# Optimization experiments

Hardware: AMD Instinct MI355X
Metric: run time of the kernel (lower is better)

## Reference

```python
import jax, jax.numpy as jnp
import numpy as np

N = 100_000          # ent_num
D = 256              # ent_dim
E_RAND = 3_200_000   # random edges (avg degree 32); + N self loops
NEG_SLOPE = 0.2      # LeakyReLU slope used by SpGraphAttentionLayer


def setup_inputs() -> dict:
    key = jax.random.key(0)
    k0, k1, k2, k3, k4, k5 = jax.random.split(key, 6)
    edges_rand = jax.random.randint(k0, (2, E_RAND), 0, N, dtype=jnp.int32)
    self_loops = jnp.tile(jnp.arange(N, dtype=jnp.int32)[None, :], (2, 1))
    edges = jnp.concatenate([edges_rand, self_loops], axis=1)  # [2, E]
    scale_w = 1.0 / np.sqrt(D).astype(np.float32)
    scale_a = 0.1 / np.sqrt(D).astype(np.float32)
    emb = jax.random.normal(k1, (N, D), jnp.float32)
    W1 = jax.random.normal(k2, (D, D), jnp.float32) * scale_w
    a1 = jax.random.normal(k3, (2 * D,), jnp.float32) * scale_a
    W2 = jax.random.normal(k4, (D, D), jnp.float32) * scale_w
    a2 = jax.random.normal(k5, (2 * D,), jnp.float32) * scale_a
    return {"emb": emb, "W1": W1, "a1": a1, "W2": W2, "a2": a2, "edges": edges}


def gat_layer(h, W, a, src, dst):
    # h: [N, D] node features; edges (src -> aggregates from dst)
    h2 = h @ W                              # [N, D]
    s_src = h2 @ a[:D]                      # [N] contribution of a . h_src
    s_dst = h2 @ a[D:]                      # [N] contribution of a . h_dst
    score = s_src[src] + s_dst[dst]         # [E] = a . [h_src; h_dst]
    e = jnp.exp(-jax.nn.leaky_relu(score, NEG_SLOPE))  # [E], pyGAT sparse form
    denom = jax.ops.segment_sum(e, src, num_segments=h.shape[0])          # [N]
    num = jax.ops.segment_sum(e[:, None] * h2[dst], src,
                              num_segments=h.shape[0])                    # [N, D]
    return jax.nn.elu(num / denom[:, None])


def reference(emb, W1, a1, W2, a2, edges):
    src, dst = edges[0], edges[1]
    h = gat_layer(emb, W1, a1, src, dst)
    h = gat_layer(h, W2, a2, src, dst)
    return h
```

## Files before the change

### kernel.cpp

```cpp
#include <hip/hip_runtime.h>
#include <hip/hip_bf16.h>

#define D 256
#define NEG_SLOPE 0.2f
#define BM 128
#define BN 128
#define BK 64
#define LDK 72

using bf16x8 = __attribute__((ext_vector_type(8))) __bf16;
using f32x4  = __attribute__((ext_vector_type(4))) float;

__device__ __forceinline__ float bf2f(unsigned short u) {
    return __uint_as_float(((unsigned int)u) << 16);
}
__device__ __forceinline__ unsigned short f2bf(float f) {
    unsigned int u = __float_as_uint(f);
    unsigned int r = (u + 0x7FFF + ((u >> 16) & 1)) >> 16;
    return (unsigned short)r;
}


__global__ void conv_bf16_kernel(const float* __restrict__ in,
                                 unsigned short* __restrict__ out, int n4) {
    int t = blockIdx.x * blockDim.x + threadIdx.x;
    if (t < n4) {
        const float4 v = *(const float4*)(in + (size_t)t * 4);
        ushort4 o;
        o.x = f2bf(v.x); o.y = f2bf(v.y); o.z = f2bf(v.z); o.w = f2bf(v.w);
        *(ushort4*)(out + (size_t)t * 4) = o;
    }
}

__global__ void transW_kernel(const float* __restrict__ W, unsigned short* __restrict__ WT) {
    const int k = blockIdx.x, n = threadIdx.x;
    WT[(size_t)n * D + k] = f2bf(W[(size_t)k * D + n]);
}


__global__ void count_kernel(const int* __restrict__ src, int* __restrict__ counts, int E) {
    int t = blockIdx.x * blockDim.x + threadIdx.x;
    if (t < E) atomicAdd(&counts[src[t]], 1);
}

__global__ __launch_bounds__(1024) void scan_kernel(const int* __restrict__ counts,
                                                    int* __restrict__ row_ptr, int n) {
    __shared__ int sums[1024];
    const int tid = threadIdx.x;
    const int chunk = (n + 1023) >> 10;
    const int beg = tid * chunk;
    const int end = min(beg + chunk, n);
    int s = 0;
    for (int i = beg; i < end; ++i) s += counts[i];
    sums[tid] = s;
    __syncthreads();
    for (int off = 1; off < 1024; off <<= 1) {
        int v = (tid >= off) ? sums[tid - off] : 0;
        __syncthreads();
        sums[tid] += v;
        __syncthreads();
    }
    int base = sums[tid] - s;
    for (int i = beg; i < end; ++i) { row_ptr[i] = base; base += counts[i]; }
    if (tid == 1023) row_ptr[n] = sums[1023];
}

__global__ void fill_kernel(const int* __restrict__ src, const int* __restrict__ dst,
                            const int* __restrict__ row_ptr, int* __restrict__ fillp,
                            int* __restrict__ col, int E) {
    int t = blockIdx.x * blockDim.x + threadIdx.x;
    if (t < E) {
        int s = src[t];
        int pos = atomicAdd(&fillp[s], 1);
        col[row_ptr[s] + pos] = dst[t];
    }
}


__global__ __launch_bounds__(256) void gemm_mfma(
    const unsigned short* __restrict__ A, const unsigned short* __restrict__ BT,
    unsigned short* __restrict__ C, int M)
{
    __shared__ unsigned short smem[2 * BM * LDK];
    unsigned short* As_ = smem;
    unsigned short* Bs_ = smem + BM * LDK;
    const int tid = threadIdx.x;
    const int m0 = blockIdx.x * BM;
    const int n0 = blockIdx.y * BN;
    const int lane = tid & 63;
    const int wv = tid >> 6;
    const int wm = (wv & 1) * 64;
    const int wn = (wv >> 1) * 64;
    const int l15 = lane & 15;
    const int quad = lane >> 4;

    f32x4 acc[4][4];
    #pragma unroll
    for (int i = 0; i < 4; ++i)
        #pragma unroll
        for (int j = 0; j < 4; ++j)
            acc[i][j] = (f32x4){0.f, 0.f, 0.f, 0.f};

    for (int k0 = 0; k0 < D; k0 += BK) {
        #pragma unroll
        for (int c = tid; c < BM * 8; c += 256) {
            const int row = c >> 3, j = c & 7;
            const int gr = m0 + row;
            uint4 av = make_uint4(0, 0, 0, 0);
            if (gr < M) av = *(const uint4*)(A + (size_t)gr * D + k0 + j * 8);
            *(uint4*)(As_ + row * LDK + j * 8) = av;
            const uint4 bv = *(const uint4*)(BT + (size_t)(n0 + row) * D + k0 + j * 8);
            *(uint4*)(Bs_ + row * LDK + j * 8) = bv;
        }
        __syncthreads();
        #pragma unroll
        for (int s = 0; s < 2; ++s) {
            bf16x8 af[4], bfr[4];
            #pragma unroll
            for (int i = 0; i < 4; ++i)
                af[i] = *(const bf16x8*)(As_ + (wm + i * 16 + l15) * LDK + s * 32 + quad * 8);
            #pragma unroll
            for (int j = 0; j < 4; ++j)
                bfr[j] = *(const bf16x8*)(Bs_ + (wn + j * 16 + l15) * LDK + s * 32 + quad * 8);
            #pragma unroll
            for (int i = 0; i < 4; ++i)
                #pragma unroll
                for (int j = 0; j < 4; ++j)
                    acc[i][j] = __builtin_amdgcn_mfma_f32_16x16x32_bf16(
                        af[i], bfr[j], acc[i][j], 0, 0, 0);
        }
        __syncthreads();
    }

    unsigned short* Cw = smem + wv * (64 * LDK);
    #pragma unroll
    for (int i = 0; i < 4; ++i)
        #pragma unroll
        for (int j = 0; j < 4; ++j)
            #pragma unroll
            for (int r = 0; r < 4; ++r)
                Cw[(i * 16 + quad * 4 + r) * LDK + j * 16 + l15] = f2bf(acc[i][j][r]);
    __syncthreads();
    #pragma unroll
    for (int rr = 0; rr < 64; rr += 2) {
        const int row = rr + (lane >> 5);
        const unsigned int wd = *(const unsigned int*)(Cw + row * LDK + (lane & 31) * 2);
        const int gr = m0 + wm + row;
        if (gr < M)
            *(unsigned int*)(C + (size_t)gr * D + n0 + wn + (lane & 31) * 2) = wd;
    }
}


__global__ __launch_bounds__(256) void score_kernel(
    const unsigned short* __restrict__ h2, const float* __restrict__ a,
    float* __restrict__ s_src, float* __restrict__ s_dst, int Nn)
{
    const int lane = threadIdx.x & 63;
    const int w = threadIdx.x >> 6;
    const int row = blockIdx.x * 4 + w;
    if (row >= Nn) return;
    const ushort4 h = *(const ushort4*)(h2 + (size_t)row * D + lane * 4);
    const float4 a1v = *(const float4*)(a + lane * 4);
    const float4 a2v = *(const float4*)(a + D + lane * 4);
    const float hx = bf2f(h.x), hy = bf2f(h.y), hz = bf2f(h.z), hw = bf2f(h.w);
    float p1 = hx * a1v.x + hy * a1v.y + hz * a1v.z + hw * a1v.w;
    float p2 = hx * a2v.x + hy * a2v.y + hz * a2v.z + hw * a2v.w;
    #pragma unroll
    for (int off = 32; off > 0; off >>= 1) {
        p1 += __shfl_down(p1, off);
        p2 += __shfl_down(p2, off);
    }
    if (lane == 0) { s_src[row] = p1; s_dst[row] = p2; }
}


__global__ __launch_bounds__(256) void agg_kernel(
    const unsigned short* __restrict__ h2, const float* __restrict__ s_src,
    const float* __restrict__ s_dst, const int* __restrict__ row_ptr,
    const int* __restrict__ col, unsigned short* __restrict__ out_bf16,
    float* __restrict__ out_f32, int Nn)
{
    const int lane = threadIdx.x & 63;
    const int node = blockIdx.x * 4 + (threadIdx.x >> 6);
    if (node >= Nn) return;
    const int beg = row_ptr[node], end = row_ptr[node + 1];
    const float ssrc = s_src[node];
    float ax = 0.f, ay = 0.f, az = 0.f, aw = 0.f;
    float dpart = 0.f;
    for (int c0 = beg; c0 < end; c0 += 64) {
        const int cnt = min(64, end - c0);
        int j = 0;
        float e = 0.f;
        if (lane < cnt) {
            j = col[c0 + lane];
            const float sc = ssrc + s_dst[j];
            const float l = sc >= 0.f ? sc : NEG_SLOPE * sc;
            e = __expf(-l);
        }
        dpart += e;
        for (int k = 0; k < cnt; ++k) {
            const float ek = __shfl(e, k);
            const int jk = __shfl(j, k);
            const ushort4 u = *(const ushort4*)(h2 + (size_t)jk * D + lane * 4);
            ax = fmaf(ek, bf2f(u.x), ax);
            ay = fmaf(ek, bf2f(u.y), ay);
            az = fmaf(ek, bf2f(u.z), az);
            aw = fmaf(ek, bf2f(u.w), aw);
        }
    }
    float denom = dpart;
    #pragma unroll
    for (int off = 32; off > 0; off >>= 1) denom += __shfl_xor(denom, off);
    const float inv = 1.f / denom;
    float vx = ax * inv, vy = ay * inv, vz = az * inv, vw = aw * inv;
    vx = vx > 0.f ? vx : expm1f(vx);
    vy = vy > 0.f ? vy : expm1f(vy);
    vz = vz > 0.f ? vz : expm1f(vz);
    vw = vw > 0.f ? vw : expm1f(vw);
    if (out_bf16) {
        ushort4 o;
        o.x = f2bf(vx); o.y = f2bf(vy); o.z = f2bf(vz); o.w = f2bf(vw);
        *(ushort4*)(out_bf16 + (size_t)node * D + lane * 4) = o;
    } else {
        *(float4*)(out_f32 + (size_t)node * D + lane * 4) = make_float4(vx, vy, vz, vw);
    }
}


static inline size_t align_up(size_t x, size_t a) { return (x + a - 1) & ~(a - 1); }

extern "C" void kernel_launch(void* const* d_in, const int* in_sizes, int n_in,
                              void* d_out, int out_size, void* d_ws, size_t ws_size,
                              hipStream_t stream)
{
    const float* emb = (const float*)d_in[0];
    const float* W1  = (const float*)d_in[1];
    const float* a1  = (const float*)d_in[2];
    const float* W2  = (const float*)d_in[3];
    const float* a2  = (const float*)d_in[4];
    const int* edges = (const int*)d_in[5];
    const int Nn = in_sizes[0] / D;
    const int E  = in_sizes[5] / 2;
    const int* src = edges;
    const int* dst = edges + E;

    size_t off = 0;
    char* base = (char*)d_ws;
    unsigned short* hA = (unsigned short*)(base + off);
    off = align_up(off + (size_t)Nn * D * sizeof(unsigned short), 256);
    unsigned short* hB = (unsigned short*)(base + off);
    off = align_up(off + (size_t)Nn * D * sizeof(unsigned short), 256);
    unsigned short* embb = (unsigned short*)(base + off);
    off = align_up(off + (size_t)Nn * D * sizeof(unsigned short), 256);
    unsigned short* WT1 = (unsigned short*)(base + off);
    off = align_up(off + (size_t)D * D * sizeof(unsigned short), 256);
    unsigned short* WT2 = (unsigned short*)(base + off);
    off = align_up(off + (size_t)D * D * sizeof(unsigned short), 256);
    float* s_src = (float*)(base + off); off = align_up(off + (size_t)Nn * sizeof(float), 256);
    float* s_dst = (float*)(base + off); off = align_up(off + (size_t)Nn * sizeof(float), 256);
    int* row_ptr = (int*)(base + off);   off = align_up(off + (size_t)(Nn + 1) * sizeof(int), 256);
    int* counts  = (int*)(base + off);   off = align_up(off + (size_t)Nn * sizeof(int), 256);
    int* fillp   = (int*)(base + off);   off = align_up(off + (size_t)Nn * sizeof(int), 256);
    int* col     = (int*)(base + off);   off = align_up(off + (size_t)E * sizeof(int), 256);

    conv_bf16_kernel<<<(Nn * D / 4 + 255) / 256, 256, 0, stream>>>(emb, embb, Nn * D / 4);
    transW_kernel<<<D, D, 0, stream>>>(W1, WT1);
    transW_kernel<<<D, D, 0, stream>>>(W2, WT2);

    hipMemsetAsync(counts, 0, (size_t)2 * align_up((size_t)Nn * sizeof(int), 256), stream);
    count_kernel<<<(E + 255) / 256, 256, 0, stream>>>(src, counts, E);
    scan_kernel<<<1, 1024, 0, stream>>>(counts, row_ptr, Nn);
    fill_kernel<<<(E + 255) / 256, 256, 0, stream>>>(src, dst, row_ptr, fillp, col, E);

    dim3 ggrid((Nn + BM - 1) / BM, D / BN);
    gemm_mfma<<<ggrid, 256, 0, stream>>>(embb, WT1, hA, Nn);
    score_kernel<<<(Nn + 3) / 4, 256, 0, stream>>>(hA, a1, s_src, s_dst, Nn);
    agg_kernel<<<(Nn + 3) / 4, 256, 0, stream>>>(hA, s_src, s_dst, row_ptr, col, hB, nullptr, Nn);
    gemm_mfma<<<ggrid, 256, 0, stream>>>(hB, WT2, hA, Nn);
    score_kernel<<<(Nn + 3) / 4, 256, 0, stream>>>(hA, a2, s_src, s_dst, Nn);
    agg_kernel<<<(Nn + 3) / 4, 256, 0, stream>>>(hA, s_src, s_dst, row_ptr, col, nullptr,
                                                 (float*)d_out, Nn);
}
```

Baseline: 1.232 ms.

## Fuse fp32-to-bf16 conversion into GEMM, parallelize CSR scan, unroll gather loop

After: 1.039 ms. -15.6%, faster.

```diff
diff --git a/kernel.cpp b/kernel.cpp
--- a/kernel.cpp
+++ b/kernel.cpp
@@ -7,6 +7,7 @@
 #define BN 128
 #define BK 64
 #define LDK 72
+#define SCAN_CHUNK 1024
 
 using bf16x8 = __attribute__((ext_vector_type(8))) __bf16;
 using f32x4  = __attribute__((ext_vector_type(4))) float;
@@ -21,17 +22,6 @@
 }
 
 
-__global__ void conv_bf16_kernel(const float* __restrict__ in,
-                                 unsigned short* __restrict__ out, int n4) {
-    int t = blockIdx.x * blockDim.x + threadIdx.x;
-    if (t < n4) {
-        const float4 v = *(const float4*)(in + (size_t)t * 4);
-        ushort4 o;
-        o.x = f2bf(v.x); o.y = f2bf(v.y); o.z = f2bf(v.z); o.w = f2bf(v.w);
-        *(ushort4*)(out + (size_t)t * 4) = o;
-    }
-}
-
 __global__ void transW_kernel(const float* __restrict__ W, unsigned short* __restrict__ WT) {
     const int k = blockIdx.x, n = threadIdx.x;
     WT[(size_t)n * D + k] = f2bf(W[(size_t)k * D + n]);
@@ -43,26 +33,81 @@
     if (t < E) atomicAdd(&counts[src[t]], 1);
 }
 
-__global__ __launch_bounds__(1024) void scan_kernel(const int* __restrict__ counts,
-                                                    int* __restrict__ row_ptr, int n) {
-    __shared__ int sums[1024];
+__global__ __launch_bounds__(256) void scan_partial_kernel(
+    const int* __restrict__ counts, int* __restrict__ partial, int n)
+{
+    __shared__ int ws[4];
     const int tid = threadIdx.x;
-    const int chunk = (n + 1023) >> 10;
-    const int beg = tid * chunk;
-    const int end = min(beg + chunk, n);
-    int s = 0;
-    for (int i = beg; i < end; ++i) s += counts[i];
-    sums[tid] = s;
+    const int lane = tid & 63, wv = tid >> 6;
+    const int idx = blockIdx.x * SCAN_CHUNK + tid * 4;
+    int4 v = make_int4(0, 0, 0, 0);
+    if (idx + 3 < n) v = *(const int4*)(counts + idx);
+    else {
+        if (idx + 0 < n) v.x = counts[idx + 0];
+        if (idx + 1 < n) v.y = counts[idx + 1];
+        if (idx + 2 < n) v.z = counts[idx + 2];
+        if (idx + 3 < n) v.w = counts[idx + 3];
+    }
+    int s = v.x + v.y + v.z + v.w;
+    #pragma unroll
+    for (int off = 32; off > 0; off >>= 1) s += __shfl_xor(s, off);
+    if (lane == 0) ws[wv] = s;
     __syncthreads();
-    for (int off = 1; off < 1024; off <<= 1) {
-        int v = (tid >= off) ? sums[tid - off] : 0;
+    if (tid == 0) partial[blockIdx.x] = ws[0] + ws[1] + ws[2] + ws[3];
+}
+
+__global__ __launch_bounds__(128) void scan_chunks_kernel(
+    const int* __restrict__ partial, int* __restrict__ chunkoff,
+    int* __restrict__ row_ptr, int nchunks, int n)
+{
+    __shared__ int sm[128];
+    const int tid = threadIdx.x;
+    const int v = (tid < nchunks) ? partial[tid] : 0;
+    sm[tid] = v;
+    __syncthreads();
+    #pragma unroll
+    for (int off = 1; off < 128; off <<= 1) {
+        int t = (tid >= off) ? sm[tid - off] : 0;
         __syncthreads();
-        sums[tid] += v;
+        sm[tid] += t;
         __syncthreads();
     }
-    int base = sums[tid] - s;
-    for (int i = beg; i < end; ++i) { row_ptr[i] = base; base += counts[i]; }
-    if (tid == 1023) row_ptr[n] = sums[1023];
+    if (tid < nchunks) chunkoff[tid] = sm[tid] - v;
+    if (tid == 127) row_ptr[n] = sm[127];
+}
+
+__global__ __launch_bounds__(256) void scan_write_kernel(
+    const int* __restrict__ counts, const int* __restrict__ chunkoff,
+    int* __restrict__ row_ptr, int n)
+{
+    __shared__ int wsum[4];
+    const int tid = threadIdx.x;
+    const int lane = tid & 63, wv = tid >> 6;
+    const int idx = blockIdx.x * SCAN_CHUNK + tid * 4;
+    int4 v = make_int4(0, 0, 0, 0);
+    if (idx + 3 < n) v = *(const int4*)(counts + idx);
+    else {
+        if (idx + 0 < n) v.x = counts[idx + 0];
+        if (idx + 1 < n) v.y = counts[idx + 1];
+        if (idx + 2 < n) v.z = counts[idx + 2];
+        if (idx + 3 < n) v.w = counts[idx + 3];
+    }
+    const int s = v.x + v.y + v.z + v.w;
+    int x = s;
+    #pragma unroll
+    for (int off = 1; off < 64; off <<= 1) {
+        int t = __shfl_up(x, off);
+        if (lane >= off) x += t;
+    }
+    if (lane == 63) wsum[wv] = x;
+    __syncthreads();
+    int wo = chunkoff[blockIdx.x];
+    for (int w = 0; w < 4; ++w) if (w < wv) wo += wsum[w];
+    int excl = wo + x - s;
+    if (idx + 0 < n) row_ptr[idx + 0] = excl;
+    if (idx + 1 < n) row_ptr[idx + 1] = excl + v.x;
+    if (idx + 2 < n) row_ptr[idx + 2] = excl + v.x + v.y;
+    if (idx + 3 < n) row_ptr[idx + 3] = excl + v.x + v.y + v.z;
 }
 
 __global__ void fill_kernel(const int* __restrict__ src, const int* __restrict__ dst,
@@ -78,7 +123,8 @@
 
 
 __global__ __launch_bounds__(256) void gemm_mfma(
-    const unsigned short* __restrict__ A, const unsigned short* __restrict__ BT,
+    const unsigned short* __restrict__ Ab, const float* __restrict__ Af,
+    const unsigned short* __restrict__ BT,
     unsigned short* __restrict__ C, int M)
 {
     __shared__ unsigned short smem[2 * BM * LDK];
@@ -107,7 +153,19 @@
             const int row = c >> 3, j = c & 7;
             const int gr = m0 + row;
             uint4 av = make_uint4(0, 0, 0, 0);
-            if (gr < M) av = *(const uint4*)(A + (size_t)gr * D + k0 + j * 8);
+            if (gr < M) {
+                if (Af) {
+                    const float* p = Af + (size_t)gr * D + k0 + j * 8;
+                    const float4 f0 = *(const float4*)p;
+                    const float4 f1 = *(const float4*)(p + 4);
+                    av.x = (unsigned int)f2bf(f0.x) | ((unsigned int)f2bf(f0.y) << 16);
+                    av.y = (unsigned int)f2bf(f0.z) | ((unsigned int)f2bf(f0.w) << 16);
+                    av.z = (unsigned int)f2bf(f1.x) | ((unsigned int)f2bf(f1.y) << 16);
+                    av.w = (unsigned int)f2bf(f1.z) | ((unsigned int)f2bf(f1.w) << 16);
+                } else {
+                    av = *(const uint4*)(Ab + (size_t)gr * D + k0 + j * 8);
+                }
+            }
             *(uint4*)(As_ + row * LDK + j * 8) = av;
             const uint4 bv = *(const uint4*)(BT + (size_t)(n0 + row) * D + k0 + j * 8);
             *(uint4*)(Bs_ + row * LDK + j * 8) = bv;
@@ -186,6 +244,7 @@
     if (node >= Nn) return;
     const int beg = row_ptr[node], end = row_ptr[node + 1];
     const float ssrc = s_src[node];
+    const unsigned short* hp = h2 + lane * 4;
     float ax = 0.f, ay = 0.f, az = 0.f, aw = 0.f;
     float dpart = 0.f;
     for (int c0 = beg; c0 < end; c0 += 64) {
@@ -199,14 +258,23 @@
             e = __expf(-l);
         }
         dpart += e;
-        for (int k = 0; k < cnt; ++k) {
-            const float ek = __shfl(e, k);
-            const int jk = __shfl(j, k);
-            const ushort4 u = *(const ushort4*)(h2 + (size_t)jk * D + lane * 4);
-            ax = fmaf(ek, bf2f(u.x), ax);
-            ay = fmaf(ek, bf2f(u.y), ay);
-            az = fmaf(ek, bf2f(u.z), az);
-            aw = fmaf(ek, bf2f(u.w), aw);
+        for (int k = 0; k < cnt; k += 4) {
+            const int   j0 = __shfl(j, k),     j1 = __shfl(j, k + 1);
+            const int   j2 = __shfl(j, k + 2), j3 = __shfl(j, k + 3);
+            const float e0 = __shfl(e, k),     e1 = __shfl(e, k + 1);
+            const float e2 = __shfl(e, k + 2), e3 = __shfl(e, k + 3);
+            const ushort4 u0 = *(const ushort4*)(hp + (size_t)j0 * D);
+            const ushort4 u1 = *(const ushort4*)(hp + (size_t)j1 * D);
+            const ushort4 u2 = *(const ushort4*)(hp + (size_t)j2 * D);
+            const ushort4 u3 = *(const ushort4*)(hp + (size_t)j3 * D);
+            ax = fmaf(e0, bf2f(u0.x), ax); ay = fmaf(e0, bf2f(u0.y), ay);
+            az = fmaf(e0, bf2f(u0.z), az); aw = fmaf(e0, bf2f(u0.w), aw);
+            ax = fmaf(e1, bf2f(u1.x), ax); ay = fmaf(e1, bf2f(u1.y), ay);
+            az = fmaf(e1, bf2f(u1.z), az); aw = fmaf(e1, bf2f(u1.w), aw);
+            ax = fmaf(e2, bf2f(u2.x), ax); ay = fmaf(e2, bf2f(u2.y), ay);
+            az = fmaf(e2, bf2f(u2.z), az); aw = fmaf(e2, bf2f(u2.w), aw);
+            ax = fmaf(e3, bf2f(u3.x), ax); ay = fmaf(e3, bf2f(u3.y), ay);
+            az = fmaf(e3, bf2f(u3.z), az); aw = fmaf(e3, bf2f(u3.w), aw);
         }
     }
     float denom = dpart;
@@ -244,14 +312,13 @@
     const int E  = in_sizes[5] / 2;
     const int* src = edges;
     const int* dst = edges + E;
+    const int nchunks = (Nn + SCAN_CHUNK - 1) / SCAN_CHUNK;
 
     size_t off = 0;
     char* base = (char*)d_ws;
     unsigned short* hA = (unsigned short*)(base + off);
     off = align_up(off + (size_t)Nn * D * sizeof(unsigned short), 256);
     unsigned short* hB = (unsigned short*)(base + off);
-    off = align_up(off + (size_t)Nn * D * sizeof(unsigned short), 256);
-    unsigned short* embb = (unsigned short*)(base + off);
     off = align_up(off + (size_t)Nn * D * sizeof(unsigned short), 256);
     unsigned short* WT1 = (unsigned short*)(base + off);
     off = align_up(off + (size_t)D * D * sizeof(unsigned short), 256);
@@ -260,24 +327,28 @@
     float* s_src = (float*)(base + off); off = align_up(off + (size_t)Nn * sizeof(float), 256);
     float* s_dst = (float*)(base + off); off = align_up(off + (size_t)Nn * sizeof(float), 256);
     int* row_ptr = (int*)(base + off);   off = align_up(off + (size_t)(Nn + 1) * sizeof(int), 256);
-    int* counts  = (int*)(base + off);   off = align_up(off + (size_t)Nn * sizeof(int), 256);
-    int* fillp   = (int*)(base + off);   off = align_up(off + (size_t)Nn * sizeof(int), 256);
+    const size_t cstride = align_up((size_t)Nn * sizeof(int), 256);
+    int* counts  = (int*)(base + off);   off += cstride;
+    int* fillp   = (int*)(base + off);   off += cstride;
+    int* partial = (int*)(base + off);   off = align_up(off + (size_t)nchunks * sizeof(int), 256);
+    int* chunkoff= (int*)(base + off);   off = align_up(off + (size_t)nchunks * sizeof(int), 256);
     int* col     = (int*)(base + off);   off = align_up(off + (size_t)E * sizeof(int), 256);
 
-    conv_bf16_kernel<<<(Nn * D / 4 + 255) / 256, 256, 0, stream>>>(emb, embb, Nn * D / 4);
     transW_kernel<<<D, D, 0, stream>>>(W1, WT1);
     transW_kernel<<<D, D, 0, stream>>>(W2, WT2);
 
-    hipMemsetAsync(counts, 0, (size_t)2 * align_up((size_t)Nn * sizeof(int), 256), stream);
+    hipMemsetAsync(counts, 0, 2 * cstride, stream);
     count_kernel<<<(E + 255) / 256, 256, 0, stream>>>(src, counts, E);
-    scan_kernel<<<1, 1024, 0, stream>>>(counts, row_ptr, Nn);
+    scan_partial_kernel<<<nchunks, 256, 0, stream>>>(counts, partial, Nn);
+    scan_chunks_kernel<<<1, 128, 0, stream>>>(partial, chunkoff, row_ptr, nchunks, Nn);
+    scan_write_kernel<<<nchunks, 256, 0, stream>>>(counts, chunkoff, row_ptr, Nn);
     fill_kernel<<<(E + 255) / 256, 256, 0, stream>>>(src, dst, row_ptr, fillp, col, E);
 
     dim3 ggrid((Nn + BM - 1) / BM, D / BN);
-    gemm_mfma<<<ggrid, 256, 0, stream>>>(embb, WT1, hA, Nn);
+    gemm_mfma<<<ggrid, 256, 0, stream>>>(nullptr, emb, WT1, hA, Nn);
     score_kernel<<<(Nn + 3) / 4, 256, 0, stream>>>(hA, a1, s_src, s_dst, Nn);
     agg_kernel<<<(Nn + 3) / 4, 256, 0, stream>>>(hA, s_src, s_dst, row_ptr, col, hB, nullptr, Nn);
-    gemm_mfma<<<ggrid, 256, 0, stream>>>(hB, WT2, hA, Nn);
+    gemm_mfma<<<ggrid, 256, 0, stream>>>(hB, nullptr, WT2, hA, Nn);
     score_kernel<<<(Nn + 3) / 4, 256, 0, stream>>>(hA, a2, s_src, s_dst, Nn);
     agg_kernel<<<(Nn + 3) / 4, 256, 0, stream>>>(hA, s_src, s_dst, row_ptr, col, nullptr,
                                                  (float*)d_out, Nn);
```
